# Optimization experiments

Measured on AMD Instinct MI355X. Metric: run time of the kernel, lower is better.

Reference implementation:

```python
import math
import jax, jax.numpy as jnp
import numpy as np

H = 1024          # hidden size
NH = 16           # num attention heads
HD = H // NH      # head dim = 64
MAXPOS = 1024
HYP_W = 0.5


def setup_inputs() -> dict:
    key = jax.random.key(0)
    ks = jax.random.split(key, 9)
    B, S = 4, 1024
    scale = 1.0 / math.sqrt(H)
    return {
        "hidden_states": jax.random.normal(ks[0], (B, S, H), jnp.float32),
        "attention_mask": jnp.zeros((B, 1, 1, S), jnp.float32),
        "hyperbolic_attention_scores": jax.random.normal(ks[1], (B, S, S), jnp.float32),
        "Wq": jax.random.normal(ks[2], (H, H), jnp.float32) * scale,
        "bq": jnp.zeros((H,), jnp.float32),
        "Wk": jax.random.normal(ks[3], (H, H), jnp.float32) * scale,
        "bk": jnp.zeros((H,), jnp.float32),
        "Wv": jax.random.normal(ks[4], (H, H), jnp.float32) * scale,
        "bv": jnp.zeros((H,), jnp.float32),
        "dist_emb": jax.random.normal(ks[5], (2 * MAXPOS - 1, HD), jnp.float32) * 0.02,
    }


def reference(hidden_states, attention_mask, hyperbolic_attention_scores,
              Wq, bq, Wk, bk, Wv, bv, dist_emb):
    B, S, _ = hidden_states.shape

    def split_heads(x):  # [B,S,H] -> [B,NH,S,HD]
        return x.reshape(B, S, NH, HD).transpose(0, 2, 1, 3)

    q = split_heads(hidden_states @ Wq + bq)
    k = split_heads(hidden_states @ Wk + bk)
    v = split_heads(hidden_states @ Wv + bv)

    # raw scores [B,NH,Sq,Sk]
    scores = jnp.einsum("bhqd,bhkd->bhqk", q, k)

    # relative_key_query position bias
    distance = jnp.arange(S)[:, None] - jnp.arange(S)[None, :]  # [Sq,Sk]
    pe = dist_emb[distance + MAXPOS - 1]                        # [Sq,Sk,HD]
    scores = scores + jnp.einsum("bhld,lrd->bhlr", q, pe)
    scores = scores + jnp.einsum("bhrd,lrd->bhlr", k, pe)

    scores = scores / math.sqrt(HD)
    scores = scores + HYP_W * hyperbolic_attention_scores[:, None, :, :]
    scores = scores + attention_mask

    probs = jax.nn.softmax(scores, axis=-1)
    ctx = jnp.einsum("bhqk,bhkd->bhqd", probs, v)  # [B,NH,S,HD]
    ctx = ctx.transpose(0, 2, 1, 3).reshape(B, S, H)
    return ctx
```

## Files before the change

kernel.cpp:

```cpp
#include <hip/hip_runtime.h>
#include <math.h>

#define S_SEQ 1024
#define NHEAD 16
#define HDIM  64
#define BATCH 4

typedef __attribute__((ext_vector_type(8))) short bf16x8;
typedef __attribute__((ext_vector_type(4))) float f32x4;

#define MFMA16 __builtin_amdgcn_mfma_f32_16x16x32_bf16

__device__ __forceinline__ float bf2f(unsigned short h) {
    union { unsigned u; float f; } un; un.u = ((unsigned)h) << 16; return un.f;
}
__device__ __forceinline__ unsigned short f2bf(float x) {
    union { float f; unsigned u; } un; un.f = x;
    unsigned r = un.u + 0x7FFFu + ((un.u >> 16) & 1u);
    return (unsigned short)(r >> 16);
}
__device__ __forceinline__ unsigned pack2bf(float a, float b) {
    return (unsigned)f2bf(a) | ((unsigned)f2bf(b) << 16);
}
__device__ __forceinline__ void glds16(const unsigned short* g, unsigned short* l) {
    __builtin_amdgcn_global_load_lds(
        (const __attribute__((address_space(1))) void*)g,
        (__attribute__((address_space(3))) void*)l, 16, 0, 0);
}

#define HS_F4 1048576
#define PE_F4 32752
#define CONV_BLKS ((HS_F4 + PE_F4 + 255) / 256)

__global__ __launch_bounds__(256) void prep_kernel(
    const float* __restrict__ hs, const float* __restrict__ de,
    const float* __restrict__ Wq, const float* __restrict__ Wk,
    const float* __restrict__ Wv,
    unsigned short* __restrict__ hsb, unsigned short* __restrict__ peb,
    unsigned short* __restrict__ wt)
{
    __shared__ float tl[64 * 67];
    const int bx = blockIdx.x;
    const int t = threadIdx.x;

    if (bx < CONV_BLKS) {
        int i = bx * 256 + t;
        if (i < HS_F4) {
            float4 v = ((const float4*)hs)[i];
            uint2 o;
            o.x = pack2bf(v.x, v.y);
            o.y = pack2bf(v.z, v.w);
            *(uint2*)(hsb + 4 * (size_t)i) = o;
        } else if (i < HS_F4 + PE_F4) {
            int j = i - HS_F4;
            float4 v = ((const float4*)de)[j];
            uint2 o;
            o.x = pack2bf(v.x, v.y);
            o.y = pack2bf(v.z, v.w);
            *(uint2*)(peb + 4 * (size_t)j) = o;
        }
        return;
    }

    const int id = bx - CONV_BLKS;
    const int which = id >> 8;
    const int rem = id & 255;
    const float* W = (which == 0) ? Wq : (which == 1) ? Wk : Wv;
    unsigned short* outp = wt + (size_t)which * 1024 * 1024;
    const int k0 = (rem >> 4) * 64, n0 = (rem & 15) * 64;

#pragma unroll
    for (int it = 0; it < 4; ++it) {
        int idx = t + it * 256;
        int kr = idx >> 4;
        int c4 = (idx & 15) << 2;
        float4 v = *(const float4*)(W + (size_t)(k0 + kr) * 1024 + n0 + c4);
        tl[kr * 67 + c4 + 0] = v.x; tl[kr * 67 + c4 + 1] = v.y;
        tl[kr * 67 + c4 + 2] = v.z; tl[kr * 67 + c4 + 3] = v.w;
    }
    __syncthreads();
#pragma unroll
    for (int it = 0; it < 2; ++it) {
        int idx = t + it * 256;
        int nr = idx >> 3;
        int k8 = (idx & 7) << 3;
        unsigned short r[8];
#pragma unroll
        for (int e = 0; e < 8; ++e) r[e] = f2bf(tl[(k8 + e) * 67 + nr]);
        uint4 o;
        o.x = (unsigned)r[0] | ((unsigned)r[1] << 16);
        o.y = (unsigned)r[2] | ((unsigned)r[3] << 16);
        o.z = (unsigned)r[4] | ((unsigned)r[5] << 16);
        o.w = (unsigned)r[6] | ((unsigned)r[7] << 16);
        *(uint4*)(outp + (size_t)(n0 + nr) * 1024 + k0 + k8) = o;
    }
}

__global__ __launch_bounds__(256, 3) void qkv_mfma_kernel(
    const unsigned short* __restrict__ hsb, const unsigned short* __restrict__ wt,
    const float* __restrict__ bq, const float* __restrict__ bk,
    const float* __restrict__ bv,
    unsigned short* __restrict__ qo, unsigned short* __restrict__ ko,
    unsigned short* __restrict__ vo)
{
    __shared__ unsigned short As[128 * 64];
    __shared__ unsigned short Bs[128 * 64];

    const int t = threadIdx.x;
    const int lane = t & 63, w = t >> 6;
    const int l16 = lane & 15, quad = lane >> 4;
    const int wm = w >> 1, wn = w & 1;
    const int lrow = lane >> 3, cs = lane & 7;
    const int n0 = blockIdx.x * 128, m0 = blockIdx.y * 128;
    const int which = blockIdx.z;
    const unsigned short* wts = wt + (size_t)which * 1024 * 1024;
    const float* bias = (which == 0) ? bq : (which == 1) ? bk : bv;

    f32x4 acc[4][4];
#pragma unroll
    for (int i = 0; i < 4; ++i)
#pragma unroll
        for (int j = 0; j < 4; ++j) acc[i][j] = (f32x4){0.f, 0.f, 0.f, 0.f};

    for (int kk = 0; kk < 1024; kk += 64) {
#pragma unroll
        for (int it = 0; it < 4; ++it) {
            int mrow = 32 * w + 8 * it + lrow;
            int kch = cs ^ (mrow & 7);
            glds16(hsb + (size_t)(m0 + mrow) * 1024 + kk + kch * 8,
                   &As[(32 * w + 8 * it) * 64]);
            glds16(wts + (size_t)(n0 + mrow) * 1024 + kk + kch * 8,
                   &Bs[(32 * w + 8 * it) * 64]);
        }
        __syncthreads();

        bf16x8 af[4][2], bf[4][2];
#pragma unroll
        for (int i = 0; i < 4; ++i) {
            int am = 64 * wm + 16 * i + l16;
            int base = am * 64;
            af[i][0] = *(bf16x8*)&As[base + ((quad ^ (am & 7)) << 3)];
            af[i][1] = *(bf16x8*)&As[base + (((quad + 4) ^ (am & 7)) << 3)];
        }
#pragma unroll
        for (int j = 0; j < 4; ++j) {
            int bn = 64 * wn + 16 * j + l16;
            int base = bn * 64;
            bf[j][0] = *(bf16x8*)&Bs[base + ((quad ^ (bn & 7)) << 3)];
            bf[j][1] = *(bf16x8*)&Bs[base + (((quad + 4) ^ (bn & 7)) << 3)];
        }
#pragma unroll
        for (int i = 0; i < 4; ++i)
#pragma unroll
            for (int j = 0; j < 4; ++j) {
                acc[i][j] = MFMA16(af[i][0], bf[j][0], acc[i][j], 0, 0, 0);
                acc[i][j] = MFMA16(af[i][1], bf[j][1], acc[i][j], 0, 0, 0);
            }
        __syncthreads();
    }

#pragma unroll
    for (int j = 0; j < 4; ++j) {
        int n = n0 + 64 * wn + 16 * j + l16;
        float bvv = bias[n];
        int hh = n >> 6, hd = n & 63;
#pragma unroll
        for (int i = 0; i < 4; ++i) {
            int mb = m0 + 64 * wm + 16 * i + 4 * quad;
            int bb = mb >> 10, s = mb & 1023;
            if (which == 2) {
                uint2 o;
                o.x = pack2bf(acc[i][j][0] + bvv, acc[i][j][1] + bvv);
                o.y = pack2bf(acc[i][j][2] + bvv, acc[i][j][3] + bvv);
                *(uint2*)(vo + ((size_t)(bb * NHEAD + hh) * HDIM + hd) * S_SEQ + s) = o;
            } else {
                unsigned short* outp = (which == 0) ? qo : ko;
#pragma unroll
                for (int r = 0; r < 4; ++r)
                    outp[((size_t)(bb * NHEAD + hh) * S_SEQ + s + r) * HDIM + hd] =
                        f2bf(acc[i][j][r] + bvv);
            }
        }
    }
}

__global__ __launch_bounds__(256, 3) void attn_mfma_kernel(
    const unsigned short* __restrict__ qw, const unsigned short* __restrict__ kw,
    const unsigned short* __restrict__ vtw, const unsigned short* __restrict__ peb,
    const float* __restrict__ hyp, const float* __restrict__ mask,
    float* __restrict__ out)
{
    __shared__ unsigned short pes[160 * 64];
    __shared__ unsigned short QDs[64 * 100];
    __shared__ unsigned short KDs[2][96 * 36];
    __shared__ unsigned short ps[64 * 32];

    const int t = threadIdx.x;
    const int lane = t & 63, w = t >> 6;
    const int l16 = lane & 15, quad = lane >> 4;
    const int lL = 16 * w + l16;
    const int l0 = blockIdx.x * 64;
    const int h = blockIdx.y, b = blockIdx.z;

    const unsigned short* qb = qw + ((size_t)(b * NHEAD + h) * S_SEQ + l0) * HDIM;
    const unsigned short* kb = kw + (size_t)(b * NHEAD + h) * S_SEQ * HDIM;
    const unsigned short* vtb = vtw + (size_t)(b * NHEAD + h) * HDIM * S_SEQ;
    const float* hypb = hyp + (size_t)b * S_SEQ * S_SEQ + (size_t)(l0 + lL) * S_SEQ;
    const float* maskb = mask + b * S_SEQ;

    const bf16x8 qf0 = *(const bf16x8*)(qb + lL * 64 + quad * 8);
    const bf16x8 qf1 = *(const bf16x8*)(qb + lL * 64 + 32 + quad * 8);

    const int pb0 = l0 + 992;
    int sbP = pb0 % 160;
    int sbQ = pb0 % 96;
    int cQ = (pb0 - lL) % 96;

    const int strow = t >> 3, stp = t & 7;
    const int swzl = (lL >> 1) & 3;

    const int fstart = (w < 2) ? 3 * w : 2 * w + 2;
    const int fcnt   = (w < 2) ? 3 : 2;

    f32x4 accO[4];
#pragma unroll
    for (int jf = 0; jf < 4; ++jf) accO[jf] = (f32x4){0.f, 0.f, 0.f, 0.f};
    float m_run = -INFINITY, lsum = 0.f;

    bf16x8 kfC0 = *(const bf16x8*)(kb + (size_t)l16 * 64 + quad * 8);
    bf16x8 kfC1 = *(const bf16x8*)(kb + (size_t)l16 * 64 + 32 + quad * 8);
    bf16x8 kfC2 = *(const bf16x8*)(kb + (size_t)(16 + l16) * 64 + quad * 8);
    bf16x8 kfC3 = *(const bf16x8*)(kb + (size_t)(16 + l16) * 64 + 32 + quad * 8);
    uint4 peReg;
    {
        int ar = pb0 - 64 + strow;
        peReg = *(const uint4*)(peb + (size_t)ar * 64 + ((stp ^ (ar & 7)) << 3));
    }

#pragma unroll
    for (int it = 0; it < 4; ++it) {
        int idx = t + it * 256;
        int row = idx >> 3, p = idx & 7;
        int ar = pb0 - 32 + row;
        int slot = ar % 160;
        int src = ar > 2046 ? 2046 : ar;
        *(uint4*)&pes[slot * 64 + (p << 3)] =
            *(const uint4*)(peb + (size_t)src * 64 + ((p ^ (slot & 7)) << 3));
    }
    __syncthreads();

#pragma unroll
    for (int jd = 0; jd < 4; ++jd) {
        int s = sbP + 32 + 16 * jd + l16; if (s >= 160) s -= 160;
        const int sw = s & 7;
        bf16x8 p0 = *(bf16x8*)&pes[s * 64 + ((quad ^ sw) << 3)];
        bf16x8 p1 = *(bf16x8*)&pes[s * 64 + (((quad + 4) ^ sw) << 3)];
        f32x4 aq = (f32x4){0.f, 0.f, 0.f, 0.f};
        aq = MFMA16(p0, qf0, aq, 0, 0, 0);
        aq = MFMA16(p1, qf1, aq, 0, 0, 0);
        int cb = cQ + 32 + 16 * jd + 4 * quad;
#pragma unroll
        for (int i = 0; i < 4; ++i) {
            int c = cb + i; if (c >= 96) c -= 96;
            QDs[lL * 100 + c] = f2bf(aq[i]);
        }
    }

    {
        unsigned short* kdp = KDs[0];
#pragma unroll
        for (int jk = 0; jk < 3; ++jk) {
            if (jk < fcnt) {
                const int f = fstart + jk;
                const int diB = 16 * ((f + 1) >> 1);
                const int rB = (f & 1) ? 0 : 16;
                int s = sbP + diB + l16; if (s >= 160) s -= 160;
                const int sw = s & 7;
                bf16x8 p0 = *(bf16x8*)&pes[s * 64 + ((quad ^ sw) << 3)];
                bf16x8 p1 = *(bf16x8*)&pes[s * 64 + (((quad + 4) ^ sw) << 3)];
                f32x4 ak = (f32x4){0.f, 0.f, 0.f, 0.f};
                if (rB == 0) {
                    ak = MFMA16(p0, kfC0, ak, 0, 0, 0);
                    ak = MFMA16(p1, kfC1, ak, 0, 0, 0);
                } else {
                    ak = MFMA16(p0, kfC2, ak, 0, 0, 0);
                    ak = MFMA16(p1, kfC3, ak, 0, 0, 0);
                }
                const int colr = rB + l16;
                const int aB = diB + colr + 4 * quad - 16;
#pragma unroll
                for (int i = 0; i < 4; ++i)
                    kdp[(aB + i) * 36 + colr] = f2bf(ak[i]);
            }
        }
    }

    for (int kt = 0; kt < 32; ++kt) {
        const int r0 = 32 * kt;
        __syncthreads();

        const float4 hv0 = *(const float4*)(hypb + r0 + 4 * quad);
        const float4 hv1 = *(const float4*)(hypb + r0 + 16 + 4 * quad);
        const float4 mv0 = *(const float4*)(maskb + r0 + 4 * quad);
        const float4 mv1 = *(const float4*)(maskb + r0 + 16 + 4 * quad);
        bf16x8 vvA[4];
#pragma unroll
        for (int jf = 0; jf < 4; ++jf)
            vvA[jf] = *(const bf16x8*)(vtb + (size_t)(16 * jf + l16) * S_SEQ +
                                       r0 + quad * 8);
        const int r0n = (kt < 31) ? r0 + 32 : r0;
        bf16x8 kfN0 = *(const bf16x8*)(kb + (size_t)(r0n + l16) * 64 + quad * 8);
        bf16x8 kfN1 = *(const bf16x8*)(kb + (size_t)(r0n + l16) * 64 + 32 + quad * 8);
        bf16x8 kfN2 = *(const bf16x8*)(kb + (size_t)(r0n + 16 + l16) * 64 + quad * 8);
        bf16x8 kfN3 = *(const bf16x8*)(kb + (size_t)(r0n + 16 + l16) * 64 + 32 + quad * 8);
        uint4 peRegN;
        {
            int ar = pb0 - r0 - 96 + strow;
            int src = ar < 0 ? 0 : ar;
            peRegN = *(const uint4*)(peb + (size_t)src * 64 + ((stp ^ (ar & 7)) << 3));
        }

        {
            int sbS = sbP - 64; if (sbS < 0) sbS += 160;
            int slot = sbS + strow; if (slot >= 160) slot -= 160;
            *(uint4*)&pes[slot * 64 + (stp << 3)] = peReg;
        }

        f32x4 accS0 = (f32x4){0.f, 0.f, 0.f, 0.f};
        f32x4 accS1 = (f32x4){0.f, 0.f, 0.f, 0.f};
        accS0 = MFMA16(kfC0, qf0, accS0, 0, 0, 0);
        accS0 = MFMA16(kfC1, qf1, accS0, 0, 0, 0);
        accS1 = MFMA16(kfC2, qf0, accS1, 0, 0, 0);
        accS1 = MFMA16(kfC3, qf1, accS1, 0, 0, 0);

#pragma unroll
        for (int jd = 0; jd < 2; ++jd) {
            int s = sbP + 16 * jd + l16; if (s >= 160) s -= 160;
            const int sw = s & 7;
            bf16x8 p0 = *(bf16x8*)&pes[s * 64 + ((quad ^ sw) << 3)];
            bf16x8 p1 = *(bf16x8*)&pes[s * 64 + (((quad + 4) ^ sw) << 3)];
            f32x4 aq = (f32x4){0.f, 0.f, 0.f, 0.f};
            aq = MFMA16(p0, qf0, aq, 0, 0, 0);
            aq = MFMA16(p1, qf1, aq, 0, 0, 0);
            int cb = cQ + 16 * jd + 4 * quad;
#pragma unroll
            for (int i = 0; i < 4; ++i) {
                int c = cb + i; if (c >= 96) c -= 96;
                QDs[lL * 100 + c] = f2bf(aq[i]);
            }
        }

        const unsigned short* kdc = KDs[kt & 1];
        float sc0[4], sc1[4];
        {
            uint2 qd2 = *(uint2*)&QDs[lL * 100 + sbQ + 28 - 4 * quad];
            uint2 kd2 = *(uint2*)&kdc[(lL + 15) * 36 + 4 * quad];
            sc0[0] = (accS0[0] + bf2f((unsigned short)(qd2.y >> 16)) +
                      bf2f((unsigned short)(kd2.x & 0xffff))) * 0.125f + 0.5f * hv0.x + mv0.x;
            sc0[1] = (accS0[1] + bf2f((unsigned short)(qd2.y & 0xffff)) +
                      bf2f((unsigned short)(kd2.x >> 16))) * 0.125f + 0.5f * hv0.y + mv0.y;
            sc0[2] = (accS0[2] + bf2f((unsigned short)(qd2.x >> 16)) +
                      bf2f((unsigned short)(kd2.y & 0xffff))) * 0.125f + 0.5f * hv0.z + mv0.z;
            sc0[3] = (accS0[3] + bf2f((unsigned short)(qd2.x & 0xffff)) +
                      bf2f((unsigned short)(kd2.y >> 16))) * 0.125f + 0.5f * hv0.w + mv0.w;
        }
        {
            uint2 qd2 = *(uint2*)&QDs[lL * 100 + sbQ + 12 - 4 * quad];
            uint2 kd2 = *(uint2*)&kdc[(lL + 15) * 36 + 16 + 4 * quad];
            sc1[0] = (accS1[0] + bf2f((unsigned short)(qd2.y >> 16)) +
                      bf2f((unsigned short)(kd2.x & 0xffff))) * 0.125f + 0.5f * hv1.x + mv1.x;
            sc1[1] = (accS1[1] + bf2f((unsigned short)(qd2.y & 0xffff)) +
                      bf2f((unsigned short)(kd2.x >> 16))) * 0.125f + 0.5f * hv1.y + mv1.y;
            sc1[2] = (accS1[2] + bf2f((unsigned short)(qd2.x >> 16)) +
                      bf2f((unsigned short)(kd2.y & 0xffff))) * 0.125f + 0.5f * hv1.z + mv1.z;
            sc1[3] = (accS1[3] + bf2f((unsigned short)(qd2.x & 0xffff)) +
                      bf2f((unsigned short)(kd2.y >> 16))) * 0.125f + 0.5f * hv1.w + mv1.w;
        }

        float mx = fmaxf(fmaxf(fmaxf(sc0[0], sc0[1]), fmaxf(sc0[2], sc0[3])),
                         fmaxf(fmaxf(sc1[0], sc1[1]), fmaxf(sc1[2], sc1[3])));
        mx = fmaxf(mx, __shfl_xor(mx, 16));
        mx = fmaxf(mx, __shfl_xor(mx, 32));
        const float m_new = fmaxf(m_run, mx);
        const float al = __expf(m_run - m_new);
        m_run = m_new;
        float rs = 0.f;
#pragma unroll
        for (int i = 0; i < 4; ++i) { sc0[i] = __expf(sc0[i] - m_new); rs += sc0[i]; }
#pragma unroll
        for (int i = 0; i < 4; ++i) { sc1[i] = __expf(sc1[i] - m_new); rs += sc1[i]; }
        rs += __shfl_xor(rs, 16);
        rs += __shfl_xor(rs, 32);
        lsum = lsum * al + rs;

        {
            uint2 pw;
            pw.x = pack2bf(sc0[0], sc0[1]); pw.y = pack2bf(sc0[2], sc0[3]);
            *(uint2*)&ps[lL * 32 + (((quad >> 1) ^ swzl) << 3) + 4 * (quad & 1)] = pw;
            pw.x = pack2bf(sc1[0], sc1[1]); pw.y = pack2bf(sc1[2], sc1[3]);
            *(uint2*)&ps[lL * 32 + (((2 + (quad >> 1)) ^ swzl) << 3) + 4 * (quad & 1)] = pw;
        }

        const bf16x8 pf = *(const bf16x8*)&ps[lL * 32 + ((quad ^ swzl) << 3)];
        const float alv0 = __shfl(al, 4 * quad + 0);
        const float alv1 = __shfl(al, 4 * quad + 1);
        const float alv2 = __shfl(al, 4 * quad + 2);
        const float alv3 = __shfl(al, 4 * quad + 3);
#pragma unroll
        for (int jf = 0; jf < 4; ++jf) {
            f32x4 o = accO[jf];
            o[0] *= alv0; o[1] *= alv1; o[2] *= alv2; o[3] *= alv3;
            o = MFMA16(pf, vvA[jf], o, 0, 0, 0);
            accO[jf] = o;
        }

        if (kt < 31) {
            unsigned short* kdp = KDs[(kt + 1) & 1];
            int sW = sbP - 32; if (sW < 0) sW += 160;
#pragma unroll
            for (int jk = 0; jk < 3; ++jk) {
                if (jk < fcnt) {
                    const int f = fstart + jk;
                    const int diB = 16 * ((f + 1) >> 1);
                    const int rB = (f & 1) ? 0 : 16;
                    int s = sW + diB + l16; if (s >= 160) s -= 160;
                    const int sw = s & 7;
                    bf16x8 p0 = *(bf16x8*)&pes[s * 64 + ((quad ^ sw) << 3)];
                    bf16x8 p1 = *(bf16x8*)&pes[s * 64 + (((quad + 4) ^ sw) << 3)];
                    f32x4 ak = (f32x4){0.f, 0.f, 0.f, 0.f};
                    if (rB == 0) {
                        ak = MFMA16(p0, kfN0, ak, 0, 0, 0);
                        ak = MFMA16(p1, kfN1, ak, 0, 0, 0);
                    } else {
                        ak = MFMA16(p0, kfN2, ak, 0, 0, 0);
                        ak = MFMA16(p1, kfN3, ak, 0, 0, 0);
                    }
                    const int colr = rB + l16;
                    const int aB = diB + colr + 4 * quad - 16;
#pragma unroll
                    for (int i = 0; i < 4; ++i)
                        kdp[(aB + i) * 36 + colr] = f2bf(ak[i]);
                }
            }
        }

        kfC0 = kfN0; kfC1 = kfN1; kfC2 = kfN2; kfC3 = kfN3;
        peReg = peRegN;
        sbP -= 32; if (sbP < 0) sbP += 160;
        sbQ -= 32; if (sbQ < 0) sbQ += 96;
        cQ -= 32; if (cQ < 0) cQ += 96;
    }

    const float ls0 = __shfl(lsum, 4 * quad + 0);
    const float ls1 = __shfl(lsum, 4 * quad + 1);
    const float ls2 = __shfl(lsum, 4 * quad + 2);
    const float ls3 = __shfl(lsum, 4 * quad + 3);
#pragma unroll
    for (int jf = 0; jf < 4; ++jf) {
        const size_t col = (size_t)h * 64 + 16 * jf + l16;
        float* ob = out + ((size_t)b * S_SEQ + l0 + 16 * w + 4 * quad) * 1024 + col;
        ob[0]        = accO[jf][0] / ls0;
        ob[1024]     = accO[jf][1] / ls1;
        ob[2048]     = accO[jf][2] / ls2;
        ob[3072]     = accO[jf][3] / ls3;
    }
}

extern "C" void kernel_launch(void* const* d_in, const int* in_sizes, int n_in,
                              void* d_out, int out_size, void* d_ws, size_t ws_size,
                              hipStream_t stream) {
    const float* hs   = (const float*)d_in[0];
    const float* mask = (const float*)d_in[1];
    const float* hyp  = (const float*)d_in[2];
    const float* Wq   = (const float*)d_in[3];
    const float* bq   = (const float*)d_in[4];
    const float* Wk   = (const float*)d_in[5];
    const float* bk   = (const float*)d_in[6];
    const float* Wv   = (const float*)d_in[7];
    const float* bv   = (const float*)d_in[8];
    const float* de   = (const float*)d_in[9];

    char* ws = (char*)d_ws;
    unsigned short* qw  = (unsigned short*)(ws);
    unsigned short* kw  = (unsigned short*)(ws + (8u << 20));
    unsigned short* vtw = (unsigned short*)(ws + (16u << 20));
    unsigned short* hsb = (unsigned short*)(ws + (24u << 20));
    unsigned short* wt  = (unsigned short*)(ws + (32u << 20));
    unsigned short* peb = (unsigned short*)(ws + (38u << 20));

    prep_kernel<<<dim3(CONV_BLKS + 768), 256, 0, stream>>>(hs, de, Wq, Wk, Wv,
                                                           hsb, peb, wt);
    qkv_mfma_kernel<<<dim3(8, 32, 3), 256, 0, stream>>>(hsb, wt, bq, bk, bv, qw, kw, vtw);
    attn_mfma_kernel<<<dim3(16, NHEAD, BATCH), 256, 0, stream>>>(
        qw, kw, vtw, peb, hyp, mask, (float*)d_out);
}
```

Measured before the change: 321.8 us.

## Restructure attention loop: single-buffered KD, smaller PE ring, prescaled Q/K

The attention loop drops the double-buffered KD tile and the software-pipelined next-K-tile precompute. Each iteration now stores the PE row, syncs, then computes QK, QD and KD for the current tile under raised wave priority, and prefetches the next K/PE after a second barrier. The PE ring shrinks to 128 rows with power-of-two masking, and launch bounds rise to 4 blocks per CU to cut LDS use and raise occupancy. The projection kernel writes Q prescaled by 1/8 via transposed MFMA operands with vectorized stores, which removes a multiply per score. The cost is an extra barrier per iteration and less overlap of the KD computation with softmax.

```diff
diff --git a/kernel.cpp b/kernel.cpp
--- a/kernel.cpp
+++ b/kernel.cpp
@@ -149,50 +149,72 @@
             bf[j][0] = *(bf16x8*)&Bs[base + ((quad ^ (bn & 7)) << 3)];
             bf[j][1] = *(bf16x8*)&Bs[base + (((quad + 4) ^ (bn & 7)) << 3)];
         }
-#pragma unroll
-        for (int i = 0; i < 4; ++i)
-#pragma unroll
-            for (int j = 0; j < 4; ++j) {
-                acc[i][j] = MFMA16(af[i][0], bf[j][0], acc[i][j], 0, 0, 0);
-                acc[i][j] = MFMA16(af[i][1], bf[j][1], acc[i][j], 0, 0, 0);
-            }
+        if (which == 2) {
+#pragma unroll
+            for (int i = 0; i < 4; ++i)
+#pragma unroll
+                for (int j = 0; j < 4; ++j) {
+                    acc[i][j] = MFMA16(af[i][0], bf[j][0], acc[i][j], 0, 0, 0);
+                    acc[i][j] = MFMA16(af[i][1], bf[j][1], acc[i][j], 0, 0, 0);
+                }
+        } else {
+#pragma unroll
+            for (int i = 0; i < 4; ++i)
+#pragma unroll
+                for (int j = 0; j < 4; ++j) {
+                    acc[i][j] = MFMA16(bf[j][0], af[i][0], acc[i][j], 0, 0, 0);
+                    acc[i][j] = MFMA16(bf[j][1], af[i][1], acc[i][j], 0, 0, 0);
+                }
+        }
         __syncthreads();
     }
 
-#pragma unroll
-    for (int j = 0; j < 4; ++j) {
-        int n = n0 + 64 * wn + 16 * j + l16;
-        float bvv = bias[n];
-        int hh = n >> 6, hd = n & 63;
-#pragma unroll
-        for (int i = 0; i < 4; ++i) {
-            int mb = m0 + 64 * wm + 16 * i + 4 * quad;
-            int bb = mb >> 10, s = mb & 1023;
-            if (which == 2) {
+    if (which == 2) {
+#pragma unroll
+        for (int j = 0; j < 4; ++j) {
+            int n = n0 + 64 * wn + 16 * j + l16;
+            float bvv = bias[n];
+            int hh = n >> 6, hd = n & 63;
+#pragma unroll
+            for (int i = 0; i < 4; ++i) {
+                int mb = m0 + 64 * wm + 16 * i + 4 * quad;
+                int bb = mb >> 10, s = mb & 1023;
                 uint2 o;
                 o.x = pack2bf(acc[i][j][0] + bvv, acc[i][j][1] + bvv);
                 o.y = pack2bf(acc[i][j][2] + bvv, acc[i][j][3] + bvv);
                 *(uint2*)(vo + ((size_t)(bb * NHEAD + hh) * HDIM + hd) * S_SEQ + s) = o;
-            } else {
-                unsigned short* outp = (which == 0) ? qo : ko;
-#pragma unroll
-                for (int r = 0; r < 4; ++r)
-                    outp[((size_t)(bb * NHEAD + hh) * S_SEQ + s + r) * HDIM + hd] =
-                        f2bf(acc[i][j][r] + bvv);
             }
         }
-    }
-}
-
-__global__ __launch_bounds__(256, 3) void attn_mfma_kernel(
+    } else {
+        unsigned short* outp = (which == 0) ? qo : ko;
+        const float qs = (which == 0) ? 0.125f : 1.0f;
+#pragma unroll
+        for (int j = 0; j < 4; ++j) {
+            int nb = n0 + 64 * wn + 16 * j + 4 * quad;
+            float4 b4 = *(const float4*)(bias + nb);
+            int hh = nb >> 6, hd = nb & 63;
+#pragma unroll
+            for (int i = 0; i < 4; ++i) {
+                int m = m0 + 64 * wm + 16 * i + l16;
+                int bb = m >> 10, s = m & 1023;
+                uint2 o;
+                o.x = pack2bf((acc[i][j][0] + b4.x) * qs, (acc[i][j][1] + b4.y) * qs);
+                o.y = pack2bf((acc[i][j][2] + b4.z) * qs, (acc[i][j][3] + b4.w) * qs);
+                *(uint2*)(outp + ((size_t)(bb * NHEAD + hh) * S_SEQ + s) * HDIM + hd) = o;
+            }
+        }
+    }
+}
+
+__global__ __launch_bounds__(256, 4) void attn_mfma_kernel(
     const unsigned short* __restrict__ qw, const unsigned short* __restrict__ kw,
     const unsigned short* __restrict__ vtw, const unsigned short* __restrict__ peb,
     const float* __restrict__ hyp, const float* __restrict__ mask,
     float* __restrict__ out)
 {
-    __shared__ unsigned short pes[160 * 64];
+    __shared__ unsigned short pes[128 * 64];
     __shared__ unsigned short QDs[64 * 100];
-    __shared__ unsigned short KDs[2][96 * 36];
+    __shared__ unsigned short KDs[96 * 36];
     __shared__ unsigned short ps[64 * 32];
 
     const int t = threadIdx.x;
@@ -212,7 +234,7 @@
     const bf16x8 qf1 = *(const bf16x8*)(qb + lL * 64 + 32 + quad * 8);
 
     const int pb0 = l0 + 992;
-    int sbP = pb0 % 160;
+    int sbP = pb0 & 127;
     int sbQ = pb0 % 96;
     int cQ = (pb0 - lL) % 96;
 
@@ -227,31 +249,21 @@
     for (int jf = 0; jf < 4; ++jf) accO[jf] = (f32x4){0.f, 0.f, 0.f, 0.f};
     float m_run = -INFINITY, lsum = 0.f;
 
-    bf16x8 kfC0 = *(const bf16x8*)(kb + (size_t)l16 * 64 + quad * 8);
-    bf16x8 kfC1 = *(const bf16x8*)(kb + (size_t)l16 * 64 + 32 + quad * 8);
-    bf16x8 kfC2 = *(const bf16x8*)(kb + (size_t)(16 + l16) * 64 + quad * 8);
-    bf16x8 kfC3 = *(const bf16x8*)(kb + (size_t)(16 + l16) * 64 + 32 + quad * 8);
-    uint4 peReg;
-    {
-        int ar = pb0 - 64 + strow;
-        peReg = *(const uint4*)(peb + (size_t)ar * 64 + ((stp ^ (ar & 7)) << 3));
-    }
-
-#pragma unroll
-    for (int it = 0; it < 4; ++it) {
+#pragma unroll
+    for (int it = 0; it < 2; ++it) {
         int idx = t + it * 256;
         int row = idx >> 3, p = idx & 7;
-        int ar = pb0 - 32 + row;
-        int slot = ar % 160;
+        int ar = pb0 + 32 + row;
+        int slot = ar & 127;
         int src = ar > 2046 ? 2046 : ar;
         *(uint4*)&pes[slot * 64 + (p << 3)] =
-            *(const uint4*)(peb + (size_t)src * 64 + ((p ^ (slot & 7)) << 3));
+            *(const uint4*)(peb + (size_t)src * 64 + ((p ^ (ar & 7)) << 3));
     }
     __syncthreads();
 
 #pragma unroll
     for (int jd = 0; jd < 4; ++jd) {
-        int s = sbP + 32 + 16 * jd + l16; if (s >= 160) s -= 160;
+        int s = (sbP + 32 + 16 * jd + l16) & 127;
         const int sw = s & 7;
         bf16x8 p0 = *(bf16x8*)&pes[s * 64 + ((quad ^ sw) << 3)];
         bf16x8 p1 = *(bf16x8*)&pes[s * 64 + (((quad + 4) ^ sw) << 3)];
@@ -266,15 +278,62 @@
         }
     }
 
+    bf16x8 kfC0 = *(const bf16x8*)(kb + (size_t)l16 * 64 + quad * 8);
+    bf16x8 kfC1 = *(const bf16x8*)(kb + (size_t)l16 * 64 + 32 + quad * 8);
+    bf16x8 kfC2 = *(const bf16x8*)(kb + (size_t)(16 + l16) * 64 + quad * 8);
+    bf16x8 kfC3 = *(const bf16x8*)(kb + (size_t)(16 + l16) * 64 + 32 + quad * 8);
+    uint4 peReg;
     {
-        unsigned short* kdp = KDs[0];
+        int ar = pb0 + strow;
+        peReg = *(const uint4*)(peb + (size_t)ar * 64 + ((stp ^ (ar & 7)) << 3));
+    }
+
+    for (int kt = 0; kt < 32; ++kt) {
+        const int r0 = 32 * kt;
+
+        const float4 hv0 = *(const float4*)(hypb + r0 + 4 * quad);
+        const float4 hv1 = *(const float4*)(hypb + r0 + 16 + 4 * quad);
+        const float4 mv0 = *(const float4*)(maskb + r0 + 4 * quad);
+        const float4 mv1 = *(const float4*)(maskb + r0 + 16 + 4 * quad);
+
+        {
+            int slot = (sbP + strow) & 127;
+            *(uint4*)&pes[slot * 64 + (stp << 3)] = peReg;
+        }
+        __syncthreads();
+
+        __builtin_amdgcn_s_setprio(1);
+        f32x4 accS0 = (f32x4){0.f, 0.f, 0.f, 0.f};
+        f32x4 accS1 = (f32x4){0.f, 0.f, 0.f, 0.f};
+        accS0 = MFMA16(kfC0, qf0, accS0, 0, 0, 0);
+        accS0 = MFMA16(kfC1, qf1, accS0, 0, 0, 0);
+        accS1 = MFMA16(kfC2, qf0, accS1, 0, 0, 0);
+        accS1 = MFMA16(kfC3, qf1, accS1, 0, 0, 0);
+
+#pragma unroll
+        for (int jd = 0; jd < 2; ++jd) {
+            int s = (sbP + 16 * jd + l16) & 127;
+            const int sw = s & 7;
+            bf16x8 p0 = *(bf16x8*)&pes[s * 64 + ((quad ^ sw) << 3)];
+            bf16x8 p1 = *(bf16x8*)&pes[s * 64 + (((quad + 4) ^ sw) << 3)];
+            f32x4 aq = (f32x4){0.f, 0.f, 0.f, 0.f};
+            aq = MFMA16(p0, qf0, aq, 0, 0, 0);
+            aq = MFMA16(p1, qf1, aq, 0, 0, 0);
+            int cb = cQ + 16 * jd + 4 * quad;
+#pragma unroll
+            for (int i = 0; i < 4; ++i) {
+                int c = cb + i; if (c >= 96) c -= 96;
+                QDs[lL * 100 + c] = f2bf(aq[i]);
+            }
+        }
+
 #pragma unroll
         for (int jk = 0; jk < 3; ++jk) {
             if (jk < fcnt) {
                 const int f = fstart + jk;
                 const int diB = 16 * ((f + 1) >> 1);
                 const int rB = (f & 1) ? 0 : 16;
-                int s = sbP + diB + l16; if (s >= 160) s -= 160;
+                int s = (sbP + diB + l16) & 127;
                 const int sw = s & 7;
                 bf16x8 p0 = *(bf16x8*)&pes[s * 64 + ((quad ^ sw) << 3)];
                 bf16x8 p1 = *(bf16x8*)&pes[s * 64 + (((quad + 4) ^ sw) << 3)];
@@ -290,91 +349,59 @@
                 const int aB = diB + colr + 4 * quad - 16;
 #pragma unroll
                 for (int i = 0; i < 4; ++i)
-                    kdp[(aB + i) * 36 + colr] = f2bf(ak[i]);
+                    KDs[(aB + i) * 36 + colr] = f2bf(ak[i] * 0.125f);
             }
         }
-    }
-
-    for (int kt = 0; kt < 32; ++kt) {
-        const int r0 = 32 * kt;
+        __builtin_amdgcn_s_setprio(0);
         __syncthreads();
 
-        const float4 hv0 = *(const float4*)(hypb + r0 + 4 * quad);
-        const float4 hv1 = *(const float4*)(hypb + r0 + 16 + 4 * quad);
-        const float4 mv0 = *(const float4*)(maskb + r0 + 4 * quad);
-        const float4 mv1 = *(const float4*)(maskb + r0 + 16 + 4 * quad);
+        {
+            const int r0n = (kt < 31) ? r0 + 32 : r0;
+            kfC0 = *(const bf16x8*)(kb + (size_t)(r0n + l16) * 64 + quad * 8);
+            kfC1 = *(const bf16x8*)(kb + (size_t)(r0n + l16) * 64 + 32 + quad * 8);
+            kfC2 = *(const bf16x8*)(kb + (size_t)(r0n + 16 + l16) * 64 + quad * 8);
+            kfC3 = *(const bf16x8*)(kb + (size_t)(r0n + 16 + l16) * 64 + 32 + quad * 8);
+            int ar = pb0 - r0n + strow;
+            peReg = *(const uint4*)(peb + (size_t)ar * 64 + ((stp ^ (ar & 7)) << 3));
+        }
         bf16x8 vvA[4];
 #pragma unroll
         for (int jf = 0; jf < 4; ++jf)
             vvA[jf] = *(const bf16x8*)(vtb + (size_t)(16 * jf + l16) * S_SEQ +
                                        r0 + quad * 8);
-        const int r0n = (kt < 31) ? r0 + 32 : r0;
-        bf16x8 kfN0 = *(const bf16x8*)(kb + (size_t)(r0n + l16) * 64 + quad * 8);
-        bf16x8 kfN1 = *(const bf16x8*)(kb + (size_t)(r0n + l16) * 64 + 32 + quad * 8);
-        bf16x8 kfN2 = *(const bf16x8*)(kb + (size_t)(r0n + 16 + l16) * 64 + quad * 8);
-        bf16x8 kfN3 = *(const bf16x8*)(kb + (size_t)(r0n + 16 + l16) * 64 + 32 + quad * 8);
-        uint4 peRegN;
-        {
-            int ar = pb0 - r0 - 96 + strow;
-            int src = ar < 0 ? 0 : ar;
-            peRegN = *(const uint4*)(peb + (size_t)src * 64 + ((stp ^ (ar & 7)) << 3));
-        }
-
-        {
-            int sbS = sbP - 64; if (sbS < 0) sbS += 160;
-            int slot = sbS + strow; if (slot >= 160) slot -= 160;
-            *(uint4*)&pes[slot * 64 + (stp << 3)] = peReg;
-        }
-
-        f32x4 accS0 = (f32x4){0.f, 0.f, 0.f, 0.f};
-        f32x4 accS1 = (f32x4){0.f, 0.f, 0.f, 0.f};
-        accS0 = MFMA16(kfC0, qf0, accS0, 0, 0, 0);
-        accS0 = MFMA16(kfC1, qf1, accS0, 0, 0, 0);
-        accS1 = MFMA16(kfC2, qf0, accS1, 0, 0, 0);
-        accS1 = MFMA16(kfC3, qf1, accS1, 0, 0, 0);
-
-#pragma unroll
-        for (int jd = 0; jd < 2; ++jd) {
-            int s = sbP + 16 * jd + l16; if (s >= 160) s -= 160;
-            const int sw = s & 7;
-            bf16x8 p0 = *(bf16x8*)&pes[s * 64 + ((quad ^ sw) << 3)];
-            bf16x8 p1 = *(bf16x8*)&pes[s * 64 + (((quad + 4) ^ sw) << 3)];
-            f32x4 aq = (f32x4){0.f, 0.f, 0.f, 0.f};
-            aq = MFMA16(p0, qf0, aq, 0, 0, 0);
-            aq = MFMA16(p1, qf1, aq, 0, 0, 0);
-            int cb = cQ + 16 * jd + 4 * quad;
-#pragma unroll
-            for (int i = 0; i < 4; ++i) {
-                int c = cb + i; if (c >= 96) c -= 96;
-                QDs[lL * 100 + c] = f2bf(aq[i]);
-            }
-        }
-
-        const unsigned short* kdc = KDs[kt & 1];
+
         float sc0[4], sc1[4];
         {
             uint2 qd2 = *(uint2*)&QDs[lL * 100 + sbQ + 28 - 4 * quad];
-            uint2 kd2 = *(uint2*)&kdc[(lL + 15) * 36 + 4 * quad];
-            sc0[0] = (accS0[0] + bf2f((unsigned short)(qd2.y >> 16)) +
-                      bf2f((unsigned short)(kd2.x & 0xffff))) * 0.125f + 0.5f * hv0.x + mv0.x;
-            sc0[1] = (accS0[1] + bf2f((unsigned short)(qd2.y & 0xffff)) +
-                      bf2f((unsigned short)(kd2.x >> 16))) * 0.125f + 0.5f * hv0.y + mv0.y;
-            sc0[2] = (accS0[2] + bf2f((unsigned short)(qd2.x >> 16)) +
-                      bf2f((unsigned short)(kd2.y & 0xffff))) * 0.125f + 0.5f * hv0.z + mv0.z;
-            sc0[3] = (accS0[3] + bf2f((unsigned short)(qd2.x & 0xffff)) +
-                      bf2f((unsigned short)(kd2.y >> 16))) * 0.125f + 0.5f * hv0.w + mv0.w;
+            uint2 kd2 = *(uint2*)&KDs[(lL + 15) * 36 + 4 * quad];
+            float hm0 = fmaf(0.5f, hv0.x, mv0.x);
+            float hm1 = fmaf(0.5f, hv0.y, mv0.y);
+            float hm2 = fmaf(0.5f, hv0.z, mv0.z);
+            float hm3 = fmaf(0.5f, hv0.w, mv0.w);
+            sc0[0] = accS0[0] + bf2f((unsigned short)(qd2.y >> 16)) +
+                     bf2f((unsigned short)(kd2.x & 0xffff)) + hm0;
+            sc0[1] = accS0[1] + bf2f((unsigned short)(qd2.y & 0xffff)) +
+                     bf2f((unsigned short)(kd2.x >> 16)) + hm1;
+            sc0[2] = accS0[2] + bf2f((unsigned short)(qd2.x >> 16)) +
+                     bf2f((unsigned short)(kd2.y & 0xffff)) + hm2;
+            sc0[3] = accS0[3] + bf2f((unsigned short)(qd2.x & 0xffff)) +
+                     bf2f((unsigned short)(kd2.y >> 16)) + hm3;
         }
         {
             uint2 qd2 = *(uint2*)&QDs[lL * 100 + sbQ + 12 - 4 * quad];
-            uint2 kd2 = *(uint2*)&kdc[(lL + 15) * 36 + 16 + 4 * quad];
-            sc1[0] = (accS1[0] + bf2f((unsigned short)(qd2.y >> 16)) +
-                      bf2f((unsigned short)(kd2.x & 0xffff))) * 0.125f + 0.5f * hv1.x + mv1.x;
-            sc1[1] = (accS1[1] + bf2f((unsigned short)(qd2.y & 0xffff)) +
-                      bf2f((unsigned short)(kd2.x >> 16))) * 0.125f + 0.5f * hv1.y + mv1.y;
-            sc1[2] = (accS1[2] + bf2f((unsigned short)(qd2.x >> 16)) +
-                      bf2f((unsigned short)(kd2.y & 0xffff))) * 0.125f + 0.5f * hv1.z + mv1.z;
-            sc1[3] = (accS1[3] + bf2f((unsigned short)(qd2.x & 0xffff)) +
-                      bf2f((unsigned short)(kd2.y >> 16))) * 0.125f + 0.5f * hv1.w + mv1.w;
+            uint2 kd2 = *(uint2*)&KDs[(lL + 15) * 36 + 16 + 4 * quad];
+            float hm0 = fmaf(0.5f, hv1.x, mv1.x);
+            float hm1 = fmaf(0.5f, hv1.y, mv1.y);
+            float hm2 = fmaf(0.5f, hv1.z, mv1.z);
+            float hm3 = fmaf(0.5f, hv1.w, mv1.w);
+            sc1[0] = accS1[0] + bf2f((unsigned short)(qd2.y >> 16)) +
+                     bf2f((unsigned short)(kd2.x & 0xffff)) + hm0;
+            sc1[1] = accS1[1] + bf2f((unsigned short)(qd2.y & 0xffff)) +
+                     bf2f((unsigned short)(kd2.x >> 16)) + hm1;
+            sc1[2] = accS1[2] + bf2f((unsigned short)(qd2.x >> 16)) +
+                     bf2f((unsigned short)(kd2.y & 0xffff)) + hm2;
+            sc1[3] = accS1[3] + bf2f((unsigned short)(qd2.x & 0xffff)) +
+                     bf2f((unsigned short)(kd2.y >> 16)) + hm3;
         }
 
         float mx = fmaxf(fmaxf(fmaxf(sc0[0], sc0[1]), fmaxf(sc0[2], sc0[3])),
@@ -414,39 +441,7 @@
             accO[jf] = o;
         }
 
-        if (kt < 31) {
-            unsigned short* kdp = KDs[(kt + 1) & 1];
-            int sW = sbP - 32; if (sW < 0) sW += 160;
-#pragma unroll
-            for (int jk = 0; jk < 3; ++jk) {
-                if (jk < fcnt) {
-                    const int f = fstart + jk;
-                    const int diB = 16 * ((f + 1) >> 1);
-                    const int rB = (f & 1) ? 0 : 16;
-                    int s = sW + diB + l16; if (s >= 160) s -= 160;
-                    const int sw = s & 7;
-                    bf16x8 p0 = *(bf16x8*)&pes[s * 64 + ((quad ^ sw) << 3)];
-                    bf16x8 p1 = *(bf16x8*)&pes[s * 64 + (((quad + 4) ^ sw) << 3)];
-                    f32x4 ak = (f32x4){0.f, 0.f, 0.f, 0.f};
-                    if (rB == 0) {
-                        ak = MFMA16(p0, kfN0, ak, 0, 0, 0);
-                        ak = MFMA16(p1, kfN1, ak, 0, 0, 0);
-                    } else {
-                        ak = MFMA16(p0, kfN2, ak, 0, 0, 0);
-                        ak = MFMA16(p1, kfN3, ak, 0, 0, 0);
-                    }
-                    const int colr = rB + l16;
-                    const int aB = diB + colr + 4 * quad - 16;
-#pragma unroll
-                    for (int i = 0; i < 4; ++i)
-                        kdp[(aB + i) * 36 + colr] = f2bf(ak[i]);
-                }
-            }
-        }
-
-        kfC0 = kfN0; kfC1 = kfN1; kfC2 = kfN2; kfC3 = kfN3;
-        peReg = peRegN;
-        sbP -= 32; if (sbP < 0) sbP += 160;
+        sbP = (sbP - 32) & 127;
         sbQ -= 32; if (sbQ < 0) sbQ += 96;
         cQ -= 32; if (cQ < 0) cQ += 96;
     }
```

Measured after the change: 483.8 us. 1.5x slower.
